# Kernel tuning notes

Measured on AMD Instinct MI355X. Metric: run time of the kernel, lower is better.

Reference implementation:

```python
import jax, jax.numpy as jnp
import numpy as np

DIM = 512
N_DAYS = 24

def setup_inputs() -> dict:
    key = jax.random.key(0)
    k1, k2, k3, k4 = jax.random.split(key, 4)
    x = jax.random.normal(k1, (64, 1024, DIM), dtype=jnp.float32)
    day_ids = jax.random.randint(k2, (64,), 0, N_DAYS, dtype=jnp.int64)
    W = jax.random.normal(k3, (N_DAYS, DIM, DIM), dtype=jnp.float32) * 0.02 + jnp.eye(DIM, dtype=jnp.float32)
    b = jax.random.normal(k4, (N_DAYS, DIM), dtype=jnp.float32) * 0.02
    return {"x": x, "day_ids": day_ids, "W": W, "b": b}

def reference(x, day_ids, W, b):
    # Gather per-sample day weights/biases, batched matmul + bias, softsign.
    # (Dropout is identity in eval mode.)
    Wd = W[day_ids]            # [B, dim, dim]
    bd = b[day_ids][:, None, :]  # [B, 1, dim]
    y = jnp.einsum('btd,bde->bte', x, Wd) + bd
    return y / (1.0 + jnp.abs(y))  # Softsign
```

## Files before the change

### kernel.cpp

```cpp
#include <hip/hip_runtime.h>


#define DIM 512
#define SEQ 1024
#define NB 64
#define NDAYS 24
#define BM 128
#define BN 128
#define BK 64
#define LDA (BK + 8)

typedef __bf16 bf16x8 __attribute__((ext_vector_type(8)));
typedef __bf16 bf16x4 __attribute__((ext_vector_type(4)));
typedef float  f32x4  __attribute__((ext_vector_type(4)));

__device__ __forceinline__ void gll16(const void* g, void* l) {
    __builtin_amdgcn_global_load_lds(
        (const __attribute__((address_space(1))) unsigned int*)g,
        (__attribute__((address_space(3))) unsigned int*)l,
        16, 0, 0);
}

__global__ __launch_bounds__(256)
void transpose_w_kernel(const float* __restrict__ W, __bf16* __restrict__ Wt) {
    __shared__ __bf16 T[32][33];
    const int d  = blockIdx.z;
    const int k0 = blockIdx.x * 32;
    const int n0 = blockIdx.y * 32;
    const int tx = threadIdx.x & 31;
    const int ty = threadIdx.x >> 5;
    const float* Wd = W + (size_t)d * DIM * DIM;
    #pragma unroll
    for (int i = 0; i < 4; ++i) {
        const int k = ty + i * 8;
        T[tx][k] = (__bf16)Wd[(size_t)(k0 + k) * DIM + n0 + tx];
    }
    __syncthreads();
    __bf16* Wtd = Wt + (size_t)d * DIM * DIM;
    #pragma unroll
    for (int i = 0; i < 4; ++i) {
        const int n = ty + i * 8;
        Wtd[(size_t)(n0 + n) * DIM + k0 + tx] = T[n][tx];
    }
}

__global__ __launch_bounds__(256, 4)
void day_adapter_kernel(const float* __restrict__ x,
                        const int*   __restrict__ day_ids,
                        const __bf16* __restrict__ Wt,
                        const float* __restrict__ bias,
                        float*       __restrict__ out)
{
    __shared__ __align__(16) __bf16 As[BM][LDA];
    __shared__ __align__(16) __bf16 Bs[BN * BK];

    const int L  = blockIdx.x;
    const int g  = (L >> 3) & 3;
    const int mb = (L & 7) | ((L >> 5) << 3);
    const int m  = mb & 7;
    const int bb = mb >> 3;

    const int n0  = g * BN;
    const int m0  = m * BM;
    const int tid = threadIdx.x;
    const int day = day_ids[bb];

    const float*  xb  = x   + (size_t)bb  * SEQ * DIM + (size_t)m0 * DIM;
    const __bf16* Wtb = Wt  + (size_t)day * DIM * DIM + (size_t)n0 * DIM;
    float*        ob  = out + (size_t)bb  * SEQ * DIM + (size_t)m0 * DIM + n0;

    const int wave = tid >> 6;
    const int lane = tid & 63;
    const int wm   = (wave >> 1) * 64;
    const int wn   = (wave & 1) * 64;
    const int l15  = lane & 15;
    const int quad = lane >> 4;
    const int kq   = quad * 8;

    const int a_row = tid >> 2;
    const int a_col = (tid & 3) * 4;

    char* BsB = (char*)Bs;

    f32x4 acc[4][4];
    const f32x4 zero = {0.f, 0.f, 0.f, 0.f};
    #pragma unroll
    for (int i = 0; i < 4; ++i)
        #pragma unroll
        for (int j = 0; j < 4; ++j) acc[i][j] = zero;

    for (int kk = 0; kk < DIM; kk += BK) {
        #pragma unroll
        for (int p = 0; p < 4; ++p) {
            const int s  = p * 256 + tid;
            const int n  = s >> 3;
            const int cp = s & 7;
            const int c  = cp ^ (n & 7);
            gll16(Wtb + (size_t)n * DIM + kk + c * 8,
                  BsB + (size_t)(p * 256 + (tid & ~63)) * 16);
        }
        #pragma unroll
        for (int h = 0; h < 2; ++h) {
            const int r = a_row + h * 64;
            #pragma unroll
            for (int i = 0; i < 4; ++i) {
                const int col = a_col + i * 16;
                const float4 f = *(const float4*)(xb + (size_t)r * DIM + kk + col);
                bf16x4 v;
                v[0] = (__bf16)f.x; v[1] = (__bf16)f.y;
                v[2] = (__bf16)f.z; v[3] = (__bf16)f.w;
                *(bf16x4*)&As[r][col] = v;
            }
        }
        __syncthreads();

        #pragma unroll
        for (int ks = 0; ks < 2; ++ks) {
            bf16x8 af[4], bfr[4];
            #pragma unroll
            for (int i = 0; i < 4; ++i)
                af[i] = *(const bf16x8*)&As[wm + i * 16 + l15][ks * 32 + kq];
            #pragma unroll
            for (int j = 0; j < 4; ++j) {
                const int n  = wn + j * 16 + l15;
                const int c  = ks * 4 + quad;
                const int cp = c ^ (n & 7);
                bfr[j] = *(const bf16x8*)&Bs[n * BK + cp * 8];
            }
            #pragma unroll
            for (int i = 0; i < 4; ++i)
                #pragma unroll
                for (int j = 0; j < 4; ++j)
                    acc[i][j] = __builtin_amdgcn_mfma_f32_16x16x32_bf16(
                        af[i], bfr[j], acc[i][j], 0, 0, 0);
        }
        __syncthreads();
    }

    float bv[4];
    #pragma unroll
    for (int j = 0; j < 4; ++j)
        bv[j] = bias[(size_t)day * DIM + n0 + wn + j * 16 + l15];

    #pragma unroll
    for (int i = 0; i < 4; ++i) {
        const int rbase = wm + i * 16 + quad * 4;
        #pragma unroll
        for (int j = 0; j < 4; ++j) {
            const int col = wn + j * 16 + l15;
            #pragma unroll
            for (int r = 0; r < 4; ++r) {
                const float y = acc[i][j][r] + bv[j];
                ob[(size_t)(rbase + r) * DIM + col] = y / (1.0f + fabsf(y));
            }
        }
    }
}

extern "C" void kernel_launch(void* const* d_in, const int* in_sizes, int n_in,
                              void* d_out, int out_size, void* d_ws, size_t ws_size,
                              hipStream_t stream) {
    const float* x       = (const float*)d_in[0];
    const int*   day_ids = (const int*)  d_in[1];
    const float* W       = (const float*)d_in[2];
    const float* bias    = (const float*)d_in[3];
    float*       out     = (float*)d_out;
    __bf16*      Wt      = (__bf16*)d_ws;

    dim3 tgrid(DIM / 32, DIM / 32, NDAYS);
    transpose_w_kernel<<<tgrid, 256, 0, stream>>>(W, Wt);

    day_adapter_kernel<<<dim3(2048), 256, 0, stream>>>(x, day_ids, Wt, bias, out);
}
```

Before: 280.3 us.

## Double-buffer B tiles and register-prefetch A tiles to overlap loads with MFMA

Adds a second LDS buffer for the weight tile so the next B tile is fetched with global_load_lds while the current one feeds MFMAs. The x tile for two steps ahead is loaded into registers and converted and stored to LDS after each compute step, with explicit waitcnt and barriers in place of __syncthreads. This is meant to hide global-memory latency behind compute. It raises register and LDS use, and occupancy is lowered to 3 waves per SIMD in launch bounds.

```diff
diff --git a/kernel.cpp b/kernel.cpp
--- a/kernel.cpp
+++ b/kernel.cpp
@@ -8,6 +8,7 @@
 #define BM 128
 #define BN 128
 #define BK 64
+#define NT (DIM / BK)
 #define LDA (BK + 8)
 
 typedef __bf16 bf16x8 __attribute__((ext_vector_type(8)));
@@ -44,7 +45,7 @@
     }
 }
 
-__global__ __launch_bounds__(256, 4)
+__global__ __launch_bounds__(256, 3)
 void day_adapter_kernel(const float* __restrict__ x,
                         const int*   __restrict__ day_ids,
                         const __bf16* __restrict__ Wt,
@@ -52,7 +53,7 @@
                         float*       __restrict__ out)
 {
     __shared__ __align__(16) __bf16 As[BM][LDA];
-    __shared__ __align__(16) __bf16 Bs[BN * BK];
+    __shared__ __align__(16) __bf16 Bs[2][BN * BK];
 
     const int L  = blockIdx.x;
     const int g  = (L >> 3) & 3;
@@ -80,8 +81,6 @@
     const int a_row = tid >> 2;
     const int a_col = (tid & 3) * 4;
 
-    char* BsB = (char*)Bs;
-
     f32x4 acc[4][4];
     const f32x4 zero = {0.f, 0.f, 0.f, 0.f};
     #pragma unroll
@@ -89,30 +88,56 @@
         #pragma unroll
         for (int j = 0; j < 4; ++j) acc[i][j] = zero;
 
-    for (int kk = 0; kk < DIM; kk += BK) {
+    float4 fA[8];
+
+    auto load_A = [&](int k0) {
+        #pragma unroll
+        for (int h = 0; h < 2; ++h)
+            #pragma unroll
+            for (int i = 0; i < 4; ++i)
+                fA[h * 4 + i] = *(const float4*)(xb + (size_t)(a_row + h * 64) * DIM
+                                                 + k0 + a_col + i * 16);
+    };
+    auto store_A = [&]() {
+        #pragma unroll
+        for (int h = 0; h < 2; ++h)
+            #pragma unroll
+            for (int i = 0; i < 4; ++i) {
+                const float4 f = fA[h * 4 + i];
+                bf16x4 v;
+                v[0] = (__bf16)f.x; v[1] = (__bf16)f.y;
+                v[2] = (__bf16)f.z; v[3] = (__bf16)f.w;
+                *(bf16x4*)&As[a_row + h * 64][a_col + i * 16] = v;
+            }
+    };
+    auto stage_B = [&](int buf, int k0) {
+        char* BsB = (char*)&Bs[buf][0];
         #pragma unroll
         for (int p = 0; p < 4; ++p) {
             const int s  = p * 256 + tid;
             const int n  = s >> 3;
             const int cp = s & 7;
             const int c  = cp ^ (n & 7);
-            gll16(Wtb + (size_t)n * DIM + kk + c * 8,
+            gll16(Wtb + (size_t)n * DIM + k0 + c * 8,
                   BsB + (size_t)(p * 256 + (tid & ~63)) * 16);
         }
-        #pragma unroll
-        for (int h = 0; h < 2; ++h) {
-            const int r = a_row + h * 64;
-            #pragma unroll
-            for (int i = 0; i < 4; ++i) {
-                const int col = a_col + i * 16;
-                const float4 f = *(const float4*)(xb + (size_t)r * DIM + kk + col);
-                bf16x4 v;
-                v[0] = (__bf16)f.x; v[1] = (__bf16)f.y;
-                v[2] = (__bf16)f.z; v[3] = (__bf16)f.w;
-                *(bf16x4*)&As[r][col] = v;
-            }
-        }
-        __syncthreads();
+    };
+
+    load_A(0);
+    stage_B(0, 0);
+    asm volatile("" ::: "memory");
+    __builtin_amdgcn_sched_barrier(0);
+    store_A();
+    load_A(BK);
+    __builtin_amdgcn_sched_barrier(0);
+    asm volatile("s_waitcnt vmcnt(8) lgkmcnt(0)" ::: "memory");
+    __builtin_amdgcn_s_barrier();
+    __builtin_amdgcn_sched_barrier(0);
+
+    #pragma unroll
+    for (int kk = 0; kk < NT; ++kk) {
+        const int cur = kk & 1;
+        if (kk < NT - 1) stage_B(cur ^ 1, (kk + 1) * BK);
 
         #pragma unroll
         for (int ks = 0; ks < 2; ++ks) {
@@ -125,7 +150,7 @@
                 const int n  = wn + j * 16 + l15;
                 const int c  = ks * 4 + quad;
                 const int cp = c ^ (n & 7);
-                bfr[j] = *(const bf16x8*)&Bs[n * BK + cp * 8];
+                bfr[j] = *(const bf16x8*)&Bs[cur][n * BK + cp * 8];
             }
             #pragma unroll
             for (int i = 0; i < 4; ++i)
@@ -134,7 +159,21 @@
                     acc[i][j] = __builtin_amdgcn_mfma_f32_16x16x32_bf16(
                         af[i], bfr[j], acc[i][j], 0, 0, 0);
         }
-        __syncthreads();
+
+        if (kk < NT - 1) {
+            __builtin_amdgcn_s_barrier();
+            asm volatile("" ::: "memory");
+            __builtin_amdgcn_sched_barrier(0);
+            store_A();
+            if (kk < NT - 2) load_A((kk + 2) * BK);
+            __builtin_amdgcn_sched_barrier(0);
+            if (kk < NT - 2)
+                asm volatile("s_waitcnt vmcnt(8) lgkmcnt(0)" ::: "memory");
+            else
+                asm volatile("s_waitcnt vmcnt(0) lgkmcnt(0)" ::: "memory");
+            __builtin_amdgcn_s_barrier();
+            __builtin_amdgcn_sched_barrier(0);
+        }
     }
 
     float bv[4];
```

After: 283.2 us. About the same (+1.0%).

## Software-pipeline GEMM K-loop with double-buffered A and triple-buffered B

Applied to the files above, without the earlier changes.

Restructures the main K loop into a software pipeline. K steps shrink to 32, the A tile is double-buffered through registers into LDS, and the B tile is triple-buffered with direct global-to-LDS loads issued two steps ahead. Each step has a single barrier, with explicit waitcnt, instead of two. Global load latency should then overlap the MFMA work, at the cost of more LDS, fewer blocks per CU (launch bounds 4 to 3), a new swizzle, and hand-tuned vmcnt counts that must match the number of loads in flight.

```diff
diff --git a/kernel.cpp b/kernel.cpp
--- a/kernel.cpp
+++ b/kernel.cpp
@@ -7,8 +7,9 @@
 #define NDAYS 24
 #define BM 128
 #define BN 128
-#define BK 64
-#define LDA (BK + 8)
+#define BK 32
+#define NT 16
+#define LDA 40
 
 typedef __bf16 bf16x8 __attribute__((ext_vector_type(8)));
 typedef __bf16 bf16x4 __attribute__((ext_vector_type(4)));
@@ -44,15 +45,15 @@
     }
 }
 
-__global__ __launch_bounds__(256, 4)
+__global__ __launch_bounds__(256, 3)
 void day_adapter_kernel(const float* __restrict__ x,
                         const int*   __restrict__ day_ids,
                         const __bf16* __restrict__ Wt,
                         const float* __restrict__ bias,
                         float*       __restrict__ out)
 {
-    __shared__ __align__(16) __bf16 As[BM][LDA];
-    __shared__ __align__(16) __bf16 Bs[BN * BK];
+    __shared__ __align__(16) __bf16 As[2][BM][LDA];
+    __shared__ __align__(16) __bf16 Bs[3][BN * BK];
 
     const int L  = blockIdx.x;
     const int g  = (L >> 3) & 3;
@@ -77,8 +78,10 @@
     const int quad = lane >> 4;
     const int kq   = quad * 8;
 
-    const int a_row = tid >> 2;
-    const int a_col = (tid & 3) * 4;
+    const int arow = tid >> 3;
+    const int acol = (tid & 7) * 4;
+    const int bn_ = tid >> 2;
+    const int bcp = tid & 3;
 
     char* BsB = (char*)Bs;
 
@@ -89,52 +92,77 @@
         #pragma unroll
         for (int j = 0; j < 4; ++j) acc[i][j] = zero;
 
-    for (int kk = 0; kk < DIM; kk += BK) {
+    float4 fA[4];
+
+    auto issueA = [&](int t) {
+        #pragma unroll
+        for (int p = 0; p < 4; ++p)
+            fA[p] = *(const float4*)(xb + (size_t)(p * 32 + arow) * DIM
+                                     + t * BK + acol);
+    };
+    auto issueB = [&](int t) {
+        char* dst = BsB + (size_t)(t % 3) * (BN * BK * 2);
+        #pragma unroll
+        for (int p = 0; p < 2; ++p) {
+            const int n = p * 64 + bn_;
+            const int c = bcp ^ (n & 3) ^ ((n >> 2) & 3);
+            gll16(Wtb + (size_t)n * DIM + t * BK + c * 8,
+                  dst + (size_t)(p * 256 + (tid & ~63)) * 16);
+        }
+    };
+    auto writeA = [&](int buf) {
         #pragma unroll
         for (int p = 0; p < 4; ++p) {
-            const int s  = p * 256 + tid;
-            const int n  = s >> 3;
-            const int cp = s & 7;
-            const int c  = cp ^ (n & 7);
-            gll16(Wtb + (size_t)n * DIM + kk + c * 8,
-                  BsB + (size_t)(p * 256 + (tid & ~63)) * 16);
-        }
-        #pragma unroll
-        for (int h = 0; h < 2; ++h) {
-            const int r = a_row + h * 64;
+            const float4 f = fA[p];
+            bf16x4 v;
+            v[0] = (__bf16)f.x; v[1] = (__bf16)f.y;
+            v[2] = (__bf16)f.z; v[3] = (__bf16)f.w;
+            *(bf16x4*)&As[buf][p * 32 + arow][acol] = v;
+        }
+    };
+
+    issueA(0);
+    issueB(0);
+    issueB(1);
+    writeA(0);
+    asm volatile("s_waitcnt vmcnt(2) lgkmcnt(0)" ::: "memory");
+    __builtin_amdgcn_sched_barrier(0);
+    __builtin_amdgcn_s_barrier();
+    __builtin_amdgcn_sched_barrier(0);
+
+    #pragma unroll
+    for (int t = 0; t < NT; ++t) {
+        const int Ac = t & 1;
+        const int Bc = t % 3;
+
+        if (t < NT - 1) issueA(t + 1);
+        if (t < NT - 2) issueB(t + 2);
+
+        bf16x8 af[4], bfr[4];
+        #pragma unroll
+        for (int i = 0; i < 4; ++i)
+            af[i] = *(const bf16x8*)&As[Ac][wm + i * 16 + l15][kq];
+        #pragma unroll
+        for (int j = 0; j < 4; ++j) {
+            const int n  = wn + j * 16 + l15;
+            const int cp = quad ^ (n & 3) ^ ((n >> 2) & 3);
+            bfr[j] = *(const bf16x8*)((const char*)&Bs[Bc][0]
+                                      + (size_t)n * 64 + cp * 16);
+        }
+        #pragma unroll
+        for (int i = 0; i < 4; ++i)
             #pragma unroll
-            for (int i = 0; i < 4; ++i) {
-                const int col = a_col + i * 16;
-                const float4 f = *(const float4*)(xb + (size_t)r * DIM + kk + col);
-                bf16x4 v;
-                v[0] = (__bf16)f.x; v[1] = (__bf16)f.y;
-                v[2] = (__bf16)f.z; v[3] = (__bf16)f.w;
-                *(bf16x4*)&As[r][col] = v;
-            }
-        }
-        __syncthreads();
-
-        #pragma unroll
-        for (int ks = 0; ks < 2; ++ks) {
-            bf16x8 af[4], bfr[4];
-            #pragma unroll
-            for (int i = 0; i < 4; ++i)
-                af[i] = *(const bf16x8*)&As[wm + i * 16 + l15][ks * 32 + kq];
-            #pragma unroll
-            for (int j = 0; j < 4; ++j) {
-                const int n  = wn + j * 16 + l15;
-                const int c  = ks * 4 + quad;
-                const int cp = c ^ (n & 7);
-                bfr[j] = *(const bf16x8*)&Bs[n * BK + cp * 8];
-            }
-            #pragma unroll
-            for (int i = 0; i < 4; ++i)
-                #pragma unroll
-                for (int j = 0; j < 4; ++j)
-                    acc[i][j] = __builtin_amdgcn_mfma_f32_16x16x32_bf16(
-                        af[i], bfr[j], acc[i][j], 0, 0, 0);
-        }
-        __syncthreads();
+            for (int j = 0; j < 4; ++j)
+                acc[i][j] = __builtin_amdgcn_mfma_f32_16x16x32_bf16(
+                    af[i], bfr[j], acc[i][j], 0, 0, 0);
+
+        if (t < NT - 1) {
+            writeA(Ac ^ 1);
+            asm volatile("s_waitcnt vmcnt(2) lgkmcnt(0)" ::: "memory");
+            __builtin_amdgcn_sched_barrier(0);
+            __builtin_amdgcn_s_barrier();
+            __builtin_amdgcn_sched_barrier(0);
+        }
     }
 
     float bv[4];
```

New measurement: 327.4 us. 1.17x slower.
